# Kernel tuning notes

Hardware: AMD Instinct MI355X
Metric: run time of the kernel (lower is better)

## Reference

```python
import jax, jax.numpy as jnp
import numpy as np

B, IN, FS, S, H = 4096, 4096, 4096, 64, 512  # batch, input_size, first_size, shape_lstm, n_hidden
D = FS // S  # per-step feature for left/right (=64); up/down per-step feature = S (=64)


def _lstm_cell(x, h, c, Wih, Whh, bih, bhh):
    # standard torch LSTMCell gate order: i, f, g, o
    g = x @ Wih.T + bih + h @ Whh.T + bhh  # (B, 4H)
    i, f, gg, o = jnp.split(g, 4, axis=-1)
    c = jax.nn.sigmoid(f) * c + jax.nn.sigmoid(i) * jnp.tanh(gg)
    h = jax.nn.sigmoid(o) * jnp.tanh(c)
    return h, c


def setup_inputs() -> dict:
    key = jax.random.key(0)
    ks = jax.random.split(key, 20)
    def cell(k, d_in):
        k1, k2, k3, k4 = jax.random.split(k, 4)
        s = 1.0 / np.sqrt(H)
        return (jax.random.uniform(k1, (4 * H, d_in), jnp.float32, -s, s),
                jax.random.uniform(k2, (4 * H, H), jnp.float32, -s, s),
                jax.random.uniform(k3, (4 * H,), jnp.float32, -s, s),
                jax.random.uniform(k4, (4 * H,), jnp.float32, -s, s))
    Wih_l, Whh_l, bih_l, bhh_l = cell(ks[0], D)
    Wih_r, Whh_r, bih_r, bhh_r = cell(ks[1], D)
    Wih_d, Whh_d, bih_d, bhh_d = cell(ks[2], S)
    return {
        "x": jax.random.normal(ks[3], (B, IN), jnp.float32),
        "h0": jax.random.normal(ks[4], (4, B, H), jnp.float32),
        "c0": jax.random.normal(ks[5], (4, B, H), jnp.float32),
        "W1": jax.random.normal(ks[6], (FS, IN), jnp.float32) * (1.0 / np.sqrt(IN)),
        "b1": jnp.zeros((FS,), jnp.float32),
        "Wih_l": Wih_l, "Whh_l": Whh_l, "bih_l": bih_l, "bhh_l": bhh_l,
        "Wih_r": Wih_r, "Whh_r": Whh_r, "bih_r": bih_r, "bhh_r": bhh_r,
        "Wih_d": Wih_d, "Whh_d": Whh_d, "bih_d": bih_d, "bhh_d": bhh_d,
        "W3": jax.random.normal(ks[7], (10, 4 * H), jnp.float32) * (1.0 / np.sqrt(4 * H)),
        "b3": jnp.zeros((10,), jnp.float32),
    }


def reference(x, h0, c0, W1, b1, Wih_l, Whh_l, bih_l, bhh_l,
              Wih_r, Whh_r, bih_r, bhh_r, Wih_d, Whh_d, bih_d, bhh_d, W3, b3):
    feat = jax.nn.relu(x @ W1.T + b1)            # (B, FS); dropout=identity (eval)
    il = feat.reshape(B, S, D)
    x_left = jnp.transpose(il, (1, 0, 2))         # (S, B, D)
    x_right = x_left[::-1]
    x_up = jnp.transpose(il, (2, 0, 1))           # (D, B, S); loop uses first S steps
    x_down = x_up[::-1]

    def step(carry, xs):
        (hl, cl, hr, cr, hu, cu, hd, cd) = carry
        xl, xr, xu, xd = xs
        hl, cl = _lstm_cell(xl, hl, cl, Wih_l, Whh_l, bih_l, bhh_l)
        hr, cr = _lstm_cell(xr, hr, cr, Wih_r, Whh_r, bih_r, bhh_r)
        # original code uses the DOWN cell for both up and down directions
        hu, cu = _lstm_cell(xu, hu, cu, Wih_d, Whh_d, bih_d, bhh_d)
        hd, cd = _lstm_cell(xd, hd, cd, Wih_d, Whh_d, bih_d, bhh_d)
        return (hl, cl, hr, cr, hu, cu, hd, cd), None

    carry0 = (h0[0], c0[0], h0[1], c0[1], h0[2], c0[2], h0[3], c0[3])
    (hl, _, hr, _, hu, _, hd, _), _ = jax.lax.scan(
        step, carry0, (x_left[:S], x_right[:S], x_up[:S], x_down[:S]))
    out = jnp.concatenate([hl, hr, hu, hd], axis=1)  # (B, 4H)
    logits = out @ W3.T + b3
    return jax.nn.log_softmax(logits, axis=1)
```

## Files before the change

### kernel.cpp

```cpp
#include <hip/hip_runtime.h>
#include <cstddef>
#include <cstdint>

namespace {

constexpr int kB  = 4096;
constexpr int kIN = 4096;
constexpr int kFS = 4096;
constexpr int kS  = 64;
constexpr int kH  = 512;
constexpr int kNG = 2048;
constexpr int kKC = 576;
constexpr int kKTiles = kKC / 32;

typedef __bf16 bf16_t;
typedef __bf16 bfrag  __attribute__((ext_vector_type(8)));
typedef __bf16 bf16v4 __attribute__((ext_vector_type(4)));
typedef float  f32x4  __attribute__((ext_vector_type(4)));

__device__ __forceinline__ void gload16(const void* g, void* l) {
  __builtin_amdgcn_global_load_lds(
      (const __attribute__((address_space(1))) void*)g,
      (__attribute__((address_space(3))) void*)l, 16, 0, 0);
}

__device__ __forceinline__ float sigf(float x) { return 1.0f / (1.0f + __expf(-x)); }
__device__ __forceinline__ float tanh_fast(float x) {
  float e = __expf(2.0f * x);
  return 1.0f - 2.0f / (e + 1.0f);
}


__global__ __launch_bounds__(256) void f2b4_kernel(const float* __restrict__ in,
                                                   bf16_t* __restrict__ out, int n4) {
  int i = blockIdx.x * 256 + threadIdx.x;
  if (i >= n4) return;
  float4 v = reinterpret_cast<const float4*>(in)[i];
  bf16v4 o = {(bf16_t)v.x, (bf16_t)v.y, (bf16_t)v.z, (bf16_t)v.w};
  *reinterpret_cast<bf16v4*>(out + (size_t)i * 4) = o;
}

__global__ __launch_bounds__(256) void pack_wcat_kernel(
    const float* __restrict__ Wih_l, const float* __restrict__ Whh_l,
    const float* __restrict__ Wih_r, const float* __restrict__ Whh_r,
    const float* __restrict__ Wih_d, const float* __restrict__ Whh_d,
    bf16_t* __restrict__ wcat) {
  int idx = blockIdx.x * 256 + threadIdx.x;
  if (idx >= 3 * kNG * kKC) return;
  int m = idx / (kNG * kKC);
  int rem = idx - m * (kNG * kKC);
  int rr = rem / kKC;
  int k  = rem - rr * kKC;
  int u = rr >> 2, g = rr & 3;
  int orow = g * kH + u;
  const float* Wih = (m == 0) ? Wih_l : (m == 1) ? Wih_r : Wih_d;
  const float* Whh = (m == 0) ? Whh_l : (m == 1) ? Whh_r : Whh_d;
  float v = (k < 64) ? Wih[(size_t)orow * 64 + k] : Whh[(size_t)orow * 512 + (k - 64)];
  wcat[idx] = (bf16_t)v;
}

__global__ __launch_bounds__(256) void pack_bias_kernel(
    const float* __restrict__ bih_l, const float* __restrict__ bhh_l,
    const float* __restrict__ bih_r, const float* __restrict__ bhh_r,
    const float* __restrict__ bih_d, const float* __restrict__ bhh_d,
    float* __restrict__ biasc) {
  int idx = blockIdx.x * 256 + threadIdx.x;
  if (idx >= 3 * kNG) return;
  int m = idx / kNG;
  int rr = idx - m * kNG;
  int u = rr >> 2, g = rr & 3;
  int orow = g * kH + u;
  const float* bi = (m == 0) ? bih_l : (m == 1) ? bih_r : bih_d;
  const float* bh = (m == 0) ? bhh_l : (m == 1) ? bhh_r : bhh_d;
  biasc[idx] = bi[orow] + bh[orow];
}

__global__ __launch_bounds__(256) void pack_hc_kernel(const float* __restrict__ h0,
                                                      const float* __restrict__ c0,
                                                      bf16_t* __restrict__ hbuf0,
                                                      float* __restrict__ cbuf, int n) {
  int i = blockIdx.x * 256 + threadIdx.x;
  if (i >= n) return;
  hbuf0[i] = (bf16_t)h0[i];
  cbuf[i]  = c0[i];
}

__global__ __launch_bounds__(256) void transpose64_kernel(const bf16_t* __restrict__ feat,
                                                          bf16_t* __restrict__ featT) {
  __shared__ bf16_t tile[64][65];
  const int b = blockIdx.x;
  const bf16_t* src = feat + (size_t)b * kFS;
  bf16_t* dst = featT + (size_t)b * kFS;
  for (int i = threadIdx.x; i < 4096; i += 256) tile[i >> 6][i & 63] = src[i];
  __syncthreads();
  for (int i = threadIdx.x; i < 4096; i += 256) dst[i] = tile[i & 63][i >> 6];
}


__global__ __launch_bounds__(256, 4) void gemm_feat_kernel(
    const bf16_t* __restrict__ X, const bf16_t* __restrict__ W,
    const float* __restrict__ b1, bf16_t* __restrict__ feat) {
  __shared__ bf16_t As[128 * 32];
  __shared__ bf16_t Bs[128 * 32];
  const int t = threadIdx.x;
  const int bid = blockIdx.x;
  const int widx = (bid & 7) * 128 + (bid >> 3);
  const int bm = widx & 31, bn = widx >> 5;
  const int w = t >> 6, l = t & 63;
  const int wm = (w >> 1) * 64, wn = (w & 1) * 64;
  const int sr = t >> 2;
  const int skS = ((t & 3) ^ ((t >> 3) & 3)) * 8;
  const int lr = l & 15;
  const int lkS = ((l >> 4) ^ ((l >> 1) & 3)) * 8;
  const int lrow4 = (l >> 4) * 4;

  f32x4 acc[4][4];
#pragma unroll
  for (int i = 0; i < 4; ++i)
#pragma unroll
    for (int j = 0; j < 4; ++j) acc[i][j] = (f32x4){0.f, 0.f, 0.f, 0.f};

  const bf16_t* ga = X + (size_t)(bm * 128 + sr) * kIN + skS;
  const bf16_t* gb = W + (size_t)(bn * 128 + sr) * kIN + skS;
  bf16_t* lA = As + w * 512;
  bf16_t* lB = Bs + w * 512;

  for (int kt = 0; kt < kIN / 32; ++kt) {
    gload16(ga, lA);
    gload16(ga + (size_t)64 * kIN, lA + 2048);
    gload16(gb, lB);
    gload16(gb + (size_t)64 * kIN, lB + 2048);
    ga += 32; gb += 32;
    __syncthreads();
    bfrag a[4], b[4];
#pragma unroll
    for (int mi = 0; mi < 4; ++mi)
      a[mi] = *reinterpret_cast<const bfrag*>(&As[(wm + mi * 16 + lr) * 32 + lkS]);
#pragma unroll
    for (int ni = 0; ni < 4; ++ni)
      b[ni] = *reinterpret_cast<const bfrag*>(&Bs[(wn + ni * 16 + lr) * 32 + lkS]);
#pragma unroll
    for (int mi = 0; mi < 4; ++mi)
#pragma unroll
      for (int ni = 0; ni < 4; ++ni)
        acc[mi][ni] = __builtin_amdgcn_mfma_f32_16x16x32_bf16(a[mi], b[ni], acc[mi][ni], 0, 0, 0);
    __syncthreads();
  }

#pragma unroll
  for (int ni = 0; ni < 4; ++ni) {
    const int col = bn * 128 + wn + ni * 16 + lr;
    const float bb = b1[col];
#pragma unroll
    for (int mi = 0; mi < 4; ++mi) {
#pragma unroll
      for (int r = 0; r < 4; ++r) {
        const int row = bm * 128 + wm + mi * 16 + lrow4 + r;
        float v = acc[mi][ni][r] + bb;
        feat[(size_t)row * kFS + col] = (bf16_t)fmaxf(v, 0.0f);
      }
    }
  }
}


__global__ __launch_bounds__(256, 4) void lstm_step_kernel(
    const bf16_t* __restrict__ feat, const bf16_t* __restrict__ featT,
    const bf16_t* __restrict__ wcat, const float* __restrict__ biasc,
    const bf16_t* __restrict__ hin, bf16_t* __restrict__ hout,
    float* __restrict__ cbuf, int s) {
  __shared__ __align__(16) unsigned char smem[32 * 132 * 4];
  bf16_t* As = (bf16_t*)smem;
  bf16_t* Bs = (bf16_t*)(smem + 8192);
  float*  Gs = (float*)smem;

  const int t = threadIdx.x;
  const int bid = blockIdx.x;
  const int widx = (bid & 7) * 256 + (bid >> 3);
  const int cell = widx >> 9;
  const int rwk  = widx & 511;
  const int bm = rwk >> 4, bn = rwk & 15;
  const int w = t >> 6, l = t & 63;
  const int wm = (w >> 1) * 64, wn = (w & 1) * 64;
  const int sr = t >> 2;
  const int skS = ((t & 3) ^ ((t >> 3) & 3)) * 8;
  const int lr = l & 15;
  const int lkS = ((l >> 4) ^ ((l >> 1) & 3)) * 8;
  const int lrow4 = (l >> 4) * 4;

  const bf16_t* xsrc = (cell < 2) ? feat : featT;
  const int off = ((cell & 1) ? (63 - s) : s) * 64;
  const int mat = (cell < 2) ? cell : 2;
  const bf16_t* Wm = wcat + (size_t)mat * kNG * kKC;
  const bf16_t* hc = hin + (size_t)cell * kB * kH;

  f32x4 acc[4][4];
#pragma unroll
  for (int i = 0; i < 4; ++i)
#pragma unroll
    for (int j = 0; j < 4; ++j) acc[i][j] = (f32x4){0.f, 0.f, 0.f, 0.f};

  const bf16_t* gax = xsrc + (size_t)(bm * 128 + sr) * kFS + off + skS;
  const bf16_t* gah = hc + (size_t)(bm * 128 + sr) * kH + skS;
  const bf16_t* gb  = Wm + (size_t)(bn * 128 + sr) * kKC + skS;
  bf16_t* lA = As + w * 512;
  bf16_t* lB = Bs + w * 512;

  for (int kt = 0; kt < kKTiles; ++kt) {
    if (kt < 2) {
      const bf16_t* ga = gax + kt * 32;
      gload16(ga, lA);
      gload16(ga + (size_t)64 * kFS, lA + 2048);
    } else {
      const bf16_t* ga = gah + (kt - 2) * 32;
      gload16(ga, lA);
      gload16(ga + (size_t)64 * kH, lA + 2048);
    }
    gload16(gb, lB);
    gload16(gb + (size_t)64 * kKC, lB + 2048);
    gb += 32;
    __syncthreads();
    bfrag a[4], b[4];
#pragma unroll
    for (int mi = 0; mi < 4; ++mi)
      a[mi] = *reinterpret_cast<const bfrag*>(&As[(wm + mi * 16 + lr) * 32 + lkS]);
#pragma unroll
    for (int ni = 0; ni < 4; ++ni)
      b[ni] = *reinterpret_cast<const bfrag*>(&Bs[(wn + ni * 16 + lr) * 32 + lkS]);
#pragma unroll
    for (int mi = 0; mi < 4; ++mi)
#pragma unroll
      for (int ni = 0; ni < 4; ++ni)
        acc[mi][ni] = __builtin_amdgcn_mfma_f32_16x16x32_bf16(a[mi], b[ni], acc[mi][ni], 0, 0, 0);
    __syncthreads();
  }

  const float* biasn = biasc + mat * kNG + bn * 128;
#pragma unroll
  for (int pass = 0; pass < 4; ++pass) {
    const int half = pass >> 1;
    const int mlo  = (pass & 1) * 2;
    if ((w >> 1) == half) {
#pragma unroll
      for (int ni = 0; ni < 4; ++ni) {
        const int colL = wn + ni * 16 + lr;
        const float bb = biasn[colL];
#pragma unroll
        for (int mi = mlo; mi < mlo + 2; ++mi)
#pragma unroll
          for (int r = 0; r < 4; ++r)
            Gs[((mi - mlo) * 16 + lrow4 + r) * 132 + colL] = acc[mi][ni][r] + bb;
      }
    }
    __syncthreads();
#pragma unroll
    for (int it = 0; it < 4; ++it) {
      const int ci = it * 256 + t;
      const int rowL = ci >> 5;
      const int u = ci & 31;
      const float4 g4 = *reinterpret_cast<const float4*>(&Gs[rowL * 132 + u * 4]);
      const float iv = sigf(g4.x);
      const float fv = sigf(g4.y);
      const float gv = tanh_fast(g4.z);
      const float ov = sigf(g4.w);
      const int batch = bm * 128 + half * 64 + mlo * 16 + rowL;
      const int unit = bn * 32 + u;
      const size_t cidx = ((size_t)cell * kB + batch) * kH + unit;
      const float cn = fv * cbuf[cidx] + iv * gv;
      cbuf[cidx] = cn;
      hout[cidx] = (bf16_t)(ov * tanh_fast(cn));
    }
    __syncthreads();
  }
}


__global__ __launch_bounds__(256) void head_kernel(const bf16_t* __restrict__ hfin,
                                                   const float* __restrict__ W3,
                                                   const float* __restrict__ b3,
                                                   float* __restrict__ out) {
  const int b = blockIdx.x, t = threadIdx.x;
  float acc[10];
#pragma unroll
  for (int j = 0; j < 10; ++j) acc[j] = 0.f;
  for (int k = t; k < 2048; k += 256) {
    const int cell = k >> 9, u = k & 511;
    const float hv = (float)hfin[((size_t)cell * kB + b) * kH + u];
#pragma unroll
    for (int j = 0; j < 10; ++j) acc[j] += hv * W3[j * 2048 + k];
  }
  __shared__ float red[256];
  __shared__ float logits[10];
  for (int j = 0; j < 10; ++j) {
    red[t] = acc[j];
    __syncthreads();
    for (int o2 = 128; o2 > 0; o2 >>= 1) {
      if (t < o2) red[t] += red[t + o2];
      __syncthreads();
    }
    if (t == 0) logits[j] = red[0] + b3[j];
    __syncthreads();
  }
  if (t == 0) {
    float mx = logits[0];
    for (int j = 1; j < 10; ++j) mx = fmaxf(mx, logits[j]);
    float se = 0.f;
    for (int j = 0; j < 10; ++j) se += expf(logits[j] - mx);
    const float lse = mx + logf(se);
    for (int j = 0; j < 10; ++j) out[(size_t)b * 10 + j] = logits[j] - lse;
  }
}

}

extern "C" void kernel_launch(void* const* d_in, const int* in_sizes, int n_in,
                              void* d_out, int out_size, void* d_ws, size_t ws_size,
                              hipStream_t stream) {
  const float* x     = (const float*)d_in[0];
  const float* h0    = (const float*)d_in[1];
  const float* c0    = (const float*)d_in[2];
  const float* W1    = (const float*)d_in[3];
  const float* b1    = (const float*)d_in[4];
  const float* Wih_l = (const float*)d_in[5];
  const float* Whh_l = (const float*)d_in[6];
  const float* bih_l = (const float*)d_in[7];
  const float* bhh_l = (const float*)d_in[8];
  const float* Wih_r = (const float*)d_in[9];
  const float* Whh_r = (const float*)d_in[10];
  const float* bih_r = (const float*)d_in[11];
  const float* bhh_r = (const float*)d_in[12];
  const float* Wih_d = (const float*)d_in[13];
  const float* Whh_d = (const float*)d_in[14];
  const float* bih_d = (const float*)d_in[15];
  const float* bhh_d = (const float*)d_in[16];
  const float* W3    = (const float*)d_in[17];
  const float* b3    = (const float*)d_in[18];
  float* out = (float*)d_out;

  char* p = (char*)d_ws;
  auto take = [&](size_t bytes) {
    char* r = p;
    p += (bytes + 255) & ~(size_t)255;
    return r;
  };
  bf16_t* xb    = (bf16_t*)take((size_t)kB * kIN * 2);
  bf16_t* w1b   = (bf16_t*)take((size_t)kFS * kIN * 2);
  bf16_t* feat  = (bf16_t*)take((size_t)kB * kFS * 2);
  bf16_t* wcat  = (bf16_t*)take((size_t)3 * kNG * kKC * 2);
  float*  biasc = (float*)take((size_t)3 * kNG * 4);
  float*  cbuf  = (float*)take((size_t)4 * kB * kH * 4);
  bf16_t* featT = xb;
  bf16_t* hbuf  = w1b;
  const size_t HSZ = (size_t)4 * kB * kH;

  f2b4_kernel<<<(kB * kIN / 4) / 256, 256, 0, stream>>>(x, xb, kB * kIN / 4);
  f2b4_kernel<<<(kFS * kIN / 4) / 256, 256, 0, stream>>>(W1, w1b, kFS * kIN / 4);
  gemm_feat_kernel<<<dim3(1024), 256, 0, stream>>>(xb, w1b, b1, feat);
  transpose64_kernel<<<kB, 256, 0, stream>>>(feat, featT);
  pack_wcat_kernel<<<(3 * kNG * kKC + 255) / 256, 256, 0, stream>>>(
      Wih_l, Whh_l, Wih_r, Whh_r, Wih_d, Whh_d, wcat);
  pack_bias_kernel<<<(3 * kNG + 255) / 256, 256, 0, stream>>>(
      bih_l, bhh_l, bih_r, bhh_r, bih_d, bhh_d, biasc);
  pack_hc_kernel<<<(int)(HSZ / 256), 256, 0, stream>>>(h0, c0, hbuf, cbuf, (int)HSZ);

  for (int s = 0; s < 64; ++s) {
    lstm_step_kernel<<<dim3(2048), 256, 0, stream>>>(
        feat, featT, wcat, biasc,
        hbuf + (size_t)(s & 1) * HSZ, hbuf + (size_t)((s + 1) & 1) * HSZ, cbuf, s);
  }
  head_kernel<<<kB, 256, 0, stream>>>(hbuf, W3, b3, out);
}
```

Measured before the change: 4.383 ms.

## Rewrite LSTM step GEMM as 256x256 tile with double-buffered LDS pipeline

Replaces the 128x128-tile, 256-thread LSTM step kernel with a 512-thread, 256x256-tile kernel. It uses K=64 slices held in double-buffered dynamic LDS (128 KB) and interleaves async global-to-LDS loads with MFMA phases, controlled by explicit waitcnt, barriers and setprio. The larger tile is meant to cut redundant weight and h traffic and hide load latency behind compute. The gate epilogue now runs per wave without block syncs. In exchange, the grid drops to 512 blocks with at most 2 per CU, and the hand-tuned vmcnt counts are fragile.

Result: faster. 4.151 ms (-5.3%).

```diff
diff --git a/kernel.cpp b/kernel.cpp
--- a/kernel.cpp
+++ b/kernel.cpp
@@ -11,7 +11,6 @@
 constexpr int kH  = 512;
 constexpr int kNG = 2048;
 constexpr int kKC = 576;
-constexpr int kKTiles = kKC / 32;
 
 typedef __bf16 bf16_t;
 typedef __bf16 bfrag  __attribute__((ext_vector_type(8)));
@@ -28,6 +27,17 @@
 __device__ __forceinline__ float tanh_fast(float x) {
   float e = __expf(2.0f * x);
   return 1.0f - 2.0f / (e + 1.0f);
+}
+
+__device__ __forceinline__ f32x4 mfma16(bfrag a, bfrag b, f32x4 c) {
+  return __builtin_amdgcn_mfma_f32_16x16x32_bf16(a, b, c, 0, 0, 0);
+}
+
+__device__ __forceinline__ void vwait(const int n) {
+  if (n == 6)      asm volatile("s_waitcnt vmcnt(6)" ::: "memory");
+  else if (n == 4) asm volatile("s_waitcnt vmcnt(4)" ::: "memory");
+  else             asm volatile("s_waitcnt vmcnt(0)" ::: "memory");
+  __builtin_amdgcn_sched_barrier(0);
 }
 
 
@@ -164,29 +174,129 @@
 }
 
 
-__global__ __launch_bounds__(256, 4) void lstm_step_kernel(
+template <class F1, class F2, class F3, class F4>
+__device__ __forceinline__ void run_tile(
+    const bf16_t* __restrict__ As_, const bf16_t* __restrict__ Bs_,
+    f32x4 (&acc)[8][4], const int wr, const int wc, const int lr, const int lq,
+    F1&& st1, F2&& st2, F3&& st3, F4&& st4,
+    const int v1, const int v2, const int v3, const int v4) {
+  bfrag a[8], b[8];
+  const int sx = lr & 7;
+
+#pragma unroll
+  for (int mm = 0; mm < 4; ++mm)
+#pragma unroll
+    for (int kk = 0; kk < 2; ++kk)
+      a[mm * 2 + kk] = *reinterpret_cast<const bfrag*>(
+          As_ + (wr * 128 + mm * 16 + lr) * 64 + (((kk * 4 + lq) ^ sx) * 8));
+#pragma unroll
+  for (int nn = 0; nn < 2; ++nn)
+#pragma unroll
+    for (int kk = 0; kk < 2; ++kk)
+      b[nn * 2 + kk] = *reinterpret_cast<const bfrag*>(
+          Bs_ + (wc * 64 + nn * 16 + lr) * 64 + (((kk * 4 + lq) ^ sx) * 8));
+  st1();
+  __builtin_amdgcn_s_barrier();
+  asm volatile("s_waitcnt lgkmcnt(0)" ::: "memory");
+  __builtin_amdgcn_sched_barrier(0);
+  __builtin_amdgcn_s_setprio(1);
+#pragma unroll
+  for (int kk = 0; kk < 2; ++kk)
+#pragma unroll
+    for (int mm = 0; mm < 4; ++mm)
+#pragma unroll
+      for (int nn = 0; nn < 2; ++nn)
+        acc[mm][nn] = mfma16(a[mm * 2 + kk], b[nn * 2 + kk], acc[mm][nn]);
+  __builtin_amdgcn_s_setprio(0);
+  __builtin_amdgcn_sched_barrier(0);
+  vwait(v1);
+  __builtin_amdgcn_s_barrier();
+
+#pragma unroll
+  for (int nn = 0; nn < 2; ++nn)
+#pragma unroll
+    for (int kk = 0; kk < 2; ++kk)
+      b[4 + nn * 2 + kk] = *reinterpret_cast<const bfrag*>(
+          Bs_ + (wc * 64 + 32 + nn * 16 + lr) * 64 + (((kk * 4 + lq) ^ sx) * 8));
+  st2();
+  __builtin_amdgcn_s_barrier();
+  asm volatile("s_waitcnt lgkmcnt(0)" ::: "memory");
+  __builtin_amdgcn_sched_barrier(0);
+  __builtin_amdgcn_s_setprio(1);
+#pragma unroll
+  for (int kk = 0; kk < 2; ++kk)
+#pragma unroll
+    for (int mm = 0; mm < 4; ++mm)
+#pragma unroll
+      for (int nn = 0; nn < 2; ++nn)
+        acc[mm][2 + nn] = mfma16(a[mm * 2 + kk], b[4 + nn * 2 + kk], acc[mm][2 + nn]);
+  __builtin_amdgcn_s_setprio(0);
+  __builtin_amdgcn_sched_barrier(0);
+  vwait(v2);
+  __builtin_amdgcn_s_barrier();
+
+#pragma unroll
+  for (int mm = 0; mm < 4; ++mm)
+#pragma unroll
+    for (int kk = 0; kk < 2; ++kk)
+      a[mm * 2 + kk] = *reinterpret_cast<const bfrag*>(
+          As_ + (wr * 128 + 64 + mm * 16 + lr) * 64 + (((kk * 4 + lq) ^ sx) * 8));
+  st3();
+  __builtin_amdgcn_s_barrier();
+  asm volatile("s_waitcnt lgkmcnt(0)" ::: "memory");
+  __builtin_amdgcn_sched_barrier(0);
+  __builtin_amdgcn_s_setprio(1);
+#pragma unroll
+  for (int kk = 0; kk < 2; ++kk)
+#pragma unroll
+    for (int mm = 0; mm < 4; ++mm)
+#pragma unroll
+      for (int nn = 0; nn < 2; ++nn)
+        acc[4 + mm][nn] = mfma16(a[mm * 2 + kk], b[nn * 2 + kk], acc[4 + mm][nn]);
+  __builtin_amdgcn_s_setprio(0);
+  __builtin_amdgcn_sched_barrier(0);
+  vwait(v3);
+  __builtin_amdgcn_s_barrier();
+
+  st4();
+  __builtin_amdgcn_s_barrier();
+  asm volatile("s_waitcnt lgkmcnt(0)" ::: "memory");
+  __builtin_amdgcn_sched_barrier(0);
+  __builtin_amdgcn_s_setprio(1);
+#pragma unroll
+  for (int kk = 0; kk < 2; ++kk)
+#pragma unroll
+    for (int mm = 0; mm < 4; ++mm)
+#pragma unroll
+      for (int nn = 0; nn < 2; ++nn)
+        acc[4 + mm][2 + nn] = mfma16(a[mm * 2 + kk], b[4 + nn * 2 + kk], acc[4 + mm][2 + nn]);
+  __builtin_amdgcn_s_setprio(0);
+  __builtin_amdgcn_sched_barrier(0);
+  vwait(v4);
+  __builtin_amdgcn_s_barrier();
+}
+
+__global__ __launch_bounds__(512, 2) void lstm_step256_kernel(
     const bf16_t* __restrict__ feat, const bf16_t* __restrict__ featT,
     const bf16_t* __restrict__ wcat, const float* __restrict__ biasc,
     const bf16_t* __restrict__ hin, bf16_t* __restrict__ hout,
     float* __restrict__ cbuf, int s) {
-  __shared__ __align__(16) unsigned char smem[32 * 132 * 4];
-  bf16_t* As = (bf16_t*)smem;
-  bf16_t* Bs = (bf16_t*)(smem + 8192);
-  float*  Gs = (float*)smem;
+  extern __shared__ __align__(16) char smem[];
+  bf16_t* Ab[2] = {(bf16_t*)smem, (bf16_t*)(smem + 65536)};
+  bf16_t* Bb[2] = {(bf16_t*)(smem + 32768), (bf16_t*)(smem + 98304)};
 
   const int t = threadIdx.x;
+  const int l = t & 63, w = t >> 6;
+  const int wr = w >> 2, wc = w & 3;
+  const int lr = l & 15, lq = l >> 4;
+  const int srow = l >> 3;
+  const int sslot = (l & 7) ^ srow;
+
   const int bid = blockIdx.x;
-  const int widx = (bid & 7) * 256 + (bid >> 3);
-  const int cell = widx >> 9;
-  const int rwk  = widx & 511;
-  const int bm = rwk >> 4, bn = rwk & 15;
-  const int w = t >> 6, l = t & 63;
-  const int wm = (w >> 1) * 64, wn = (w & 1) * 64;
-  const int sr = t >> 2;
-  const int skS = ((t & 3) ^ ((t >> 3) & 3)) * 8;
-  const int lr = l & 15;
-  const int lkS = ((l >> 4) ^ ((l >> 1) & 3)) * 8;
-  const int lrow4 = (l >> 4) * 4;
+  const int widx = (bid & 7) * 64 + (bid >> 3);
+  const int cell = widx >> 7;
+  const int rwk = widx & 127;
+  const int bm = rwk >> 3, bn = rwk & 7;
 
   const bf16_t* xsrc = (cell < 2) ? feat : featT;
   const int off = ((cell & 1) ? (63 - s) : s) * 64;
@@ -194,83 +304,93 @@
   const bf16_t* Wm = wcat + (size_t)mat * kNG * kKC;
   const bf16_t* hc = hin + (size_t)cell * kB * kH;
 
-  f32x4 acc[4][4];
-#pragma unroll
-  for (int i = 0; i < 4; ++i)
+  auto stage_A = [&](int kt, bf16_t* dstA, int ra) {
+#pragma unroll
+    for (int j = 0; j < 2; ++j) {
+      const int row0 = ra * 64 + w * 8 + j * 128;
+      bf16_t* dst = dstA + row0 * 64;
+      const bf16_t* src = (kt == 0)
+          ? xsrc + (size_t)(bm * 256 + row0 + srow) * kFS + off + sslot * 8
+          : hc + (size_t)(bm * 256 + row0 + srow) * kH + (kt - 1) * 64 + sslot * 8;
+      gload16(src, dst);
+    }
+  };
+  auto stage_B = [&](int kt, bf16_t* dstB, int rb) {
+#pragma unroll
+    for (int j = 0; j < 2; ++j) {
+      const int row0 = (w >> 2) * 64 + (w & 3) * 8 + rb * 32 + j * 128;
+      bf16_t* dst = dstB + row0 * 64;
+      const bf16_t* src =
+          Wm + (size_t)(bn * 256 + row0 + srow) * kKC + kt * 64 + sslot * 8;
+      gload16(src, dst);
+    }
+  };
+
+  f32x4 acc[8][4];
+#pragma unroll
+  for (int i = 0; i < 8; ++i)
 #pragma unroll
     for (int j = 0; j < 4; ++j) acc[i][j] = (f32x4){0.f, 0.f, 0.f, 0.f};
 
-  const bf16_t* gax = xsrc + (size_t)(bm * 128 + sr) * kFS + off + skS;
-  const bf16_t* gah = hc + (size_t)(bm * 128 + sr) * kH + skS;
-  const bf16_t* gb  = Wm + (size_t)(bn * 128 + sr) * kKC + skS;
-  bf16_t* lA = As + w * 512;
-  bf16_t* lB = Bs + w * 512;
-
-  for (int kt = 0; kt < kKTiles; ++kt) {
-    if (kt < 2) {
-      const bf16_t* ga = gax + kt * 32;
-      gload16(ga, lA);
-      gload16(ga + (size_t)64 * kFS, lA + 2048);
-    } else {
-      const bf16_t* ga = gah + (kt - 2) * 32;
-      gload16(ga, lA);
-      gload16(ga + (size_t)64 * kH, lA + 2048);
-    }
-    gload16(gb, lB);
-    gload16(gb + (size_t)64 * kKC, lB + 2048);
-    gb += 32;
-    __syncthreads();
-    bfrag a[4], b[4];
-#pragma unroll
-    for (int mi = 0; mi < 4; ++mi)
-      a[mi] = *reinterpret_cast<const bfrag*>(&As[(wm + mi * 16 + lr) * 32 + lkS]);
-#pragma unroll
-    for (int ni = 0; ni < 4; ++ni)
-      b[ni] = *reinterpret_cast<const bfrag*>(&Bs[(wn + ni * 16 + lr) * 32 + lkS]);
-#pragma unroll
-    for (int mi = 0; mi < 4; ++mi)
-#pragma unroll
-      for (int ni = 0; ni < 4; ++ni)
-        acc[mi][ni] = __builtin_amdgcn_mfma_f32_16x16x32_bf16(a[mi], b[ni], acc[mi][ni], 0, 0, 0);
-    __syncthreads();
-  }
-
-  const float* biasn = biasc + mat * kNG + bn * 128;
-#pragma unroll
-  for (int pass = 0; pass < 4; ++pass) {
-    const int half = pass >> 1;
-    const int mlo  = (pass & 1) * 2;
-    if ((w >> 1) == half) {
-#pragma unroll
-      for (int ni = 0; ni < 4; ++ni) {
-        const int colL = wn + ni * 16 + lr;
-        const float bb = biasn[colL];
-#pragma unroll
-        for (int mi = mlo; mi < mlo + 2; ++mi)
-#pragma unroll
-          for (int r = 0; r < 4; ++r)
-            Gs[((mi - mlo) * 16 + lrow4 + r) * 132 + colL] = acc[mi][ni][r] + bb;
-      }
-    }
-    __syncthreads();
-#pragma unroll
-    for (int it = 0; it < 4; ++it) {
-      const int ci = it * 256 + t;
-      const int rowL = ci >> 5;
-      const int u = ci & 31;
-      const float4 g4 = *reinterpret_cast<const float4*>(&Gs[rowL * 132 + u * 4]);
+  stage_A(0, Ab[0], 0); stage_B(0, Bb[0], 0);
+  stage_A(0, Ab[0], 1); stage_B(0, Bb[0], 1);
+  stage_A(1, Ab[1], 0); stage_B(1, Bb[1], 0);
+  vwait(4);
+  __builtin_amdgcn_s_barrier();
+
+  run_tile(Ab[0], Bb[0], acc, wr, wc, lr, lq,
+           [&] { stage_A(1, Ab[1], 1); }, [&] { stage_B(1, Bb[1], 1); },
+           [&] { stage_A(2, Ab[0], 0); }, [&] { stage_B(2, Bb[0], 0); },
+           6, 6, 6, 6);
+
+  for (int S = 1; S <= 5; S += 2) {
+    run_tile(Ab[1], Bb[1], acc, wr, wc, lr, lq,
+             [&] { stage_A(S + 1, Ab[0], 1); }, [&] { stage_B(S + 1, Bb[0], 1); },
+             [&] { stage_A(S + 2, Ab[1], 0); }, [&] { stage_B(S + 2, Bb[1], 0); },
+             6, 6, 6, 6);
+    run_tile(Ab[0], Bb[0], acc, wr, wc, lr, lq,
+             [&] { stage_A(S + 2, Ab[1], 1); }, [&] { stage_B(S + 2, Bb[1], 1); },
+             [&] { stage_A(S + 3, Ab[0], 0); }, [&] { stage_B(S + 3, Bb[0], 0); },
+             6, 6, 6, 6);
+  }
+  run_tile(Ab[1], Bb[1], acc, wr, wc, lr, lq,
+           [&] { stage_A(8, Ab[0], 1); }, [&] { stage_B(8, Bb[0], 1); },
+           [&] {}, [&] {}, 6, 6, 6, 4);
+  run_tile(Ab[0], Bb[0], acc, wr, wc, lr, lq,
+           [&] {}, [&] {}, [&] {}, [&] {}, 0, 0, 0, 0);
+
+  float* Gw = (float*)smem + w * 2176;
+  const float* biasn = biasc + mat * kNG + bn * 256 + wc * 64;
+  float bb[4];
+#pragma unroll
+  for (int n = 0; n < 4; ++n) bb[n] = biasn[n * 16 + lr];
+  const int rowg0 = bm * 256 + wr * 128;
+  const int unit = bn * 64 + wc * 16 + lr;
+#pragma unroll
+  for (int ch = 0; ch < 4; ++ch) {
+#pragma unroll
+    for (int mm = 0; mm < 2; ++mm) {
+      const int m = ch * 2 + mm;
+#pragma unroll
+      for (int n = 0; n < 4; ++n)
+#pragma unroll
+        for (int j = 0; j < 4; ++j)
+          Gw[(mm * 16 + lq * 4 + j) * 68 + n * 16 + lr] = acc[m][n][j] + bb[n];
+    }
+#pragma unroll
+    for (int rr = 0; rr < 8; ++rr) {
+      const int row = rr * 4 + lq;
+      const float4 g4 = *reinterpret_cast<const float4*>(&Gw[row * 68 + lr * 4]);
       const float iv = sigf(g4.x);
       const float fv = sigf(g4.y);
       const float gv = tanh_fast(g4.z);
       const float ov = sigf(g4.w);
-      const int batch = bm * 128 + half * 64 + mlo * 16 + rowL;
-      const int unit = bn * 32 + u;
-      const size_t cidx = ((size_t)cell * kB + batch) * kH + unit;
+      const int grow = rowg0 + ch * 32 + row;
+      const size_t cidx = ((size_t)cell * kB + grow) * kH + unit;
       const float cn = fv * cbuf[cidx] + iv * gv;
       cbuf[cidx] = cn;
       hout[cidx] = (bf16_t)(ov * tanh_fast(cn));
     }
-    __syncthreads();
   }
 }
 
@@ -353,6 +473,9 @@
   bf16_t* hbuf  = w1b;
   const size_t HSZ = (size_t)4 * kB * kH;
 
+  (void)hipFuncSetAttribute(reinterpret_cast<const void*>(&lstm_step256_kernel),
+                            hipFuncAttributeMaxDynamicSharedMemorySize, 131072);
+
   f2b4_kernel<<<(kB * kIN / 4) / 256, 256, 0, stream>>>(x, xb, kB * kIN / 4);
   f2b4_kernel<<<(kFS * kIN / 4) / 256, 256, 0, stream>>>(W1, w1b, kFS * kIN / 4);
   gemm_feat_kernel<<<dim3(1024), 256, 0, stream>>>(xb, w1b, b1, feat);
@@ -364,7 +487,7 @@
   pack_hc_kernel<<<(int)(HSZ / 256), 256, 0, stream>>>(h0, c0, hbuf, cbuf, (int)HSZ);
 
   for (int s = 0; s < 64; ++s) {
-    lstm_step_kernel<<<dim3(2048), 256, 0, stream>>>(
+    lstm_step256_kernel<<<dim3(512), 512, 131072, stream>>>(
         feat, featT, wcat, biasc,
         hbuf + (size_t)(s & 1) * HSZ, hbuf + (size_t)((s + 1) & 1) * HSZ, cbuf, s);
   }
```

## Double-buffer LSTM step GEMM with 64-wide K tiles and per-wave epilogue

Applied to the files above, without the earlier changes.

The LSTM step kernel now stages 64-wide K tiles into two 32KB LDS buffers, so the next tile's global-to-LDS loads run during the current tile's MFMAs. This halves the number of K iterations and barriers, and raises MFMA priority with setprio. The gate epilogue now goes through a per-wave LDS region instead of four block-wide passes with syncs. The head kernel's reduction is replaced with wave shuffles. The cost is 64KB of dynamic LDS per block, which lowers occupancy to about 2 blocks per CU.

Result: faster. 4.118 ms (-6.1%).

```diff
diff --git a/kernel.cpp b/kernel.cpp
--- a/kernel.cpp
+++ b/kernel.cpp
@@ -11,7 +11,6 @@
 constexpr int kH  = 512;
 constexpr int kNG = 2048;
 constexpr int kKC = 576;
-constexpr int kKTiles = kKC / 32;
 
 typedef __bf16 bf16_t;
 typedef __bf16 bfrag  __attribute__((ext_vector_type(8)));
@@ -28,6 +27,10 @@
 __device__ __forceinline__ float tanh_fast(float x) {
   float e = __expf(2.0f * x);
   return 1.0f - 2.0f / (e + 1.0f);
+}
+
+__device__ __forceinline__ f32x4 mfma16(bfrag a, bfrag b, f32x4 c) {
+  return __builtin_amdgcn_mfma_f32_16x16x32_bf16(a, b, c, 0, 0, 0);
 }
 
 
@@ -164,29 +167,26 @@
 }
 
 
-__global__ __launch_bounds__(256, 4) void lstm_step_kernel(
+__global__ __launch_bounds__(256, 2) void lstm_step128_kernel(
     const bf16_t* __restrict__ feat, const bf16_t* __restrict__ featT,
     const bf16_t* __restrict__ wcat, const float* __restrict__ biasc,
     const bf16_t* __restrict__ hin, bf16_t* __restrict__ hout,
     float* __restrict__ cbuf, int s) {
-  __shared__ __align__(16) unsigned char smem[32 * 132 * 4];
-  bf16_t* As = (bf16_t*)smem;
-  bf16_t* Bs = (bf16_t*)(smem + 8192);
-  float*  Gs = (float*)smem;
+  extern __shared__ __align__(16) char smem[];
 
   const int t = threadIdx.x;
+  const int l = t & 63, w = t >> 6;
+  const int wm = (w >> 1) * 64, wn = (w & 1) * 64;
+  const int lr = l & 15, lq = l >> 4;
+  const int sx = lr & 7;
+  const int srow = l >> 3;
+  const int sslot = (l & 7) ^ srow;
+
   const int bid = blockIdx.x;
   const int widx = (bid & 7) * 256 + (bid >> 3);
   const int cell = widx >> 9;
-  const int rwk  = widx & 511;
+  const int rwk = widx & 511;
   const int bm = rwk >> 4, bn = rwk & 15;
-  const int w = t >> 6, l = t & 63;
-  const int wm = (w >> 1) * 64, wn = (w & 1) * 64;
-  const int sr = t >> 2;
-  const int skS = ((t & 3) ^ ((t >> 3) & 3)) * 8;
-  const int lr = l & 15;
-  const int lkS = ((l >> 4) ^ ((l >> 1) & 3)) * 8;
-  const int lrow4 = (l >> 4) * 4;
 
   const bf16_t* xsrc = (cell < 2) ? feat : featT;
   const int off = ((cell & 1) ? (63 - s) : s) * 64;
@@ -194,83 +194,101 @@
   const bf16_t* Wm = wcat + (size_t)mat * kNG * kKC;
   const bf16_t* hc = hin + (size_t)cell * kB * kH;
 
+  auto stage = [&](int kt, int buf) {
+    char* base = smem + buf * 32768;
+#pragma unroll
+    for (int j = 0; j < 4; ++j) {
+      const int row0 = j * 32 + w * 8;
+      bf16_t* dst = (bf16_t*)base + row0 * 64;
+      const bf16_t* src = (kt == 0)
+          ? xsrc + (size_t)(bm * 128 + row0 + srow) * kFS + off + sslot * 8
+          : hc + (size_t)(bm * 128 + row0 + srow) * kH + (kt - 1) * 64 + sslot * 8;
+      gload16(src, dst);
+    }
+#pragma unroll
+    for (int j = 0; j < 4; ++j) {
+      const int row0 = j * 32 + w * 8;
+      bf16_t* dst = (bf16_t*)(base + 16384) + row0 * 64;
+      const bf16_t* src =
+          Wm + (size_t)(bn * 128 + row0 + srow) * kKC + kt * 64 + sslot * 8;
+      gload16(src, dst);
+    }
+  };
+
   f32x4 acc[4][4];
 #pragma unroll
   for (int i = 0; i < 4; ++i)
 #pragma unroll
     for (int j = 0; j < 4; ++j) acc[i][j] = (f32x4){0.f, 0.f, 0.f, 0.f};
 
-  const bf16_t* gax = xsrc + (size_t)(bm * 128 + sr) * kFS + off + skS;
-  const bf16_t* gah = hc + (size_t)(bm * 128 + sr) * kH + skS;
-  const bf16_t* gb  = Wm + (size_t)(bn * 128 + sr) * kKC + skS;
-  bf16_t* lA = As + w * 512;
-  bf16_t* lB = Bs + w * 512;
-
-  for (int kt = 0; kt < kKTiles; ++kt) {
-    if (kt < 2) {
-      const bf16_t* ga = gax + kt * 32;
-      gload16(ga, lA);
-      gload16(ga + (size_t)64 * kFS, lA + 2048);
-    } else {
-      const bf16_t* ga = gah + (kt - 2) * 32;
-      gload16(ga, lA);
-      gload16(ga + (size_t)64 * kH, lA + 2048);
-    }
-    gload16(gb, lB);
-    gload16(gb + (size_t)64 * kKC, lB + 2048);
-    gb += 32;
-    __syncthreads();
-    bfrag a[4], b[4];
+  stage(0, 0);
+  asm volatile("s_waitcnt vmcnt(0)" ::: "memory");
+  __builtin_amdgcn_sched_barrier(0);
+  __builtin_amdgcn_s_barrier();
+
+  for (int kt = 0; kt < 9; ++kt) {
+    const int cur = kt & 1;
+    if (kt < 8) stage(kt + 1, cur ^ 1);
+    const bf16_t* As_ = (const bf16_t*)(smem + cur * 32768);
+    const bf16_t* Bs_ = (const bf16_t*)(smem + cur * 32768 + 16384);
+    bfrag a[8], b[8];
 #pragma unroll
     for (int mi = 0; mi < 4; ++mi)
-      a[mi] = *reinterpret_cast<const bfrag*>(&As[(wm + mi * 16 + lr) * 32 + lkS]);
+#pragma unroll
+      for (int kk = 0; kk < 2; ++kk)
+        a[mi * 2 + kk] = *reinterpret_cast<const bfrag*>(
+            As_ + (wm + mi * 16 + lr) * 64 + (((kk * 4 + lq) ^ sx) * 8));
 #pragma unroll
     for (int ni = 0; ni < 4; ++ni)
-      b[ni] = *reinterpret_cast<const bfrag*>(&Bs[(wn + ni * 16 + lr) * 32 + lkS]);
-#pragma unroll
-    for (int mi = 0; mi < 4; ++mi)
-#pragma unroll
-      for (int ni = 0; ni < 4; ++ni)
-        acc[mi][ni] = __builtin_amdgcn_mfma_f32_16x16x32_bf16(a[mi], b[ni], acc[mi][ni], 0, 0, 0);
-    __syncthreads();
-  }
-
-  const float* biasn = biasc + mat * kNG + bn * 128;
-#pragma unroll
-  for (int pass = 0; pass < 4; ++pass) {
-    const int half = pass >> 1;
-    const int mlo  = (pass & 1) * 2;
-    if ((w >> 1) == half) {
-#pragma unroll
-      for (int ni = 0; ni < 4; ++ni) {
-        const int colL = wn + ni * 16 + lr;
-        const float bb = biasn[colL];
-#pragma unroll
-        for (int mi = mlo; mi < mlo + 2; ++mi)
-#pragma unroll
-          for (int r = 0; r < 4; ++r)
-            Gs[((mi - mlo) * 16 + lrow4 + r) * 132 + colL] = acc[mi][ni][r] + bb;
-      }
-    }
-    __syncthreads();
+#pragma unroll
+      for (int kk = 0; kk < 2; ++kk)
+        b[ni * 2 + kk] = *reinterpret_cast<const bfrag*>(
+            Bs_ + (wn + ni * 16 + lr) * 64 + (((kk * 4 + lq) ^ sx) * 8));
+    __builtin_amdgcn_s_setprio(1);
+#pragma unroll
+    for (int kk = 0; kk < 2; ++kk)
+#pragma unroll
+      for (int mi = 0; mi < 4; ++mi)
+#pragma unroll
+        for (int ni = 0; ni < 4; ++ni)
+          acc[mi][ni] = mfma16(a[mi * 2 + kk], b[ni * 2 + kk], acc[mi][ni]);
+    __builtin_amdgcn_s_setprio(0);
+    __builtin_amdgcn_sched_barrier(0);
+    asm volatile("s_waitcnt vmcnt(0)" ::: "memory");
+    __builtin_amdgcn_sched_barrier(0);
+    __builtin_amdgcn_s_barrier();
+  }
+
+  float* Gw = (float*)(smem + 32768 + w * 4352);
+  const float* biasn = biasc + mat * kNG + bn * 128 + wn;
+  float bb[4];
+#pragma unroll
+  for (int n = 0; n < 4; ++n) bb[n] = biasn[n * 16 + lr];
+  const int rowg0 = bm * 128 + wm;
+  const int unit0 = bn * 32 + (w & 1) * 16;
+#pragma unroll
+  for (int mi = 0; mi < 4; ++mi) {
+#pragma unroll
+    for (int n = 0; n < 4; ++n)
+#pragma unroll
+      for (int j = 0; j < 4; ++j)
+        Gw[(lq * 4 + j) * 68 + n * 16 + lr] = acc[mi][n][j] + bb[n];
 #pragma unroll
     for (int it = 0; it < 4; ++it) {
-      const int ci = it * 256 + t;
-      const int rowL = ci >> 5;
-      const int u = ci & 31;
-      const float4 g4 = *reinterpret_cast<const float4*>(&Gs[rowL * 132 + u * 4]);
+      const int item = it * 64 + l;
+      const int row = item >> 4;
+      const int u = item & 15;
+      const float4 g4 = *reinterpret_cast<const float4*>(&Gw[row * 68 + u * 4]);
       const float iv = sigf(g4.x);
       const float fv = sigf(g4.y);
       const float gv = tanh_fast(g4.z);
       const float ov = sigf(g4.w);
-      const int batch = bm * 128 + half * 64 + mlo * 16 + rowL;
-      const int unit = bn * 32 + u;
-      const size_t cidx = ((size_t)cell * kB + batch) * kH + unit;
+      const int grow = rowg0 + mi * 16 + row;
+      const size_t cidx = ((size_t)cell * kB + grow) * kH + unit0 + u;
       const float cn = fv * cbuf[cidx] + iv * gv;
       cbuf[cidx] = cn;
       hout[cidx] = (bf16_t)(ov * tanh_fast(cn));
     }
-    __syncthreads();
   }
 }
 
@@ -280,6 +298,7 @@
                                                    const float* __restrict__ b3,
                                                    float* __restrict__ out) {
   const int b = blockIdx.x, t = threadIdx.x;
+  const int l = t & 63, w = t >> 6;
   float acc[10];
 #pragma unroll
   for (int j = 0; j < 10; ++j) acc[j] = 0.f;
@@ -289,24 +308,28 @@
 #pragma unroll
     for (int j = 0; j < 10; ++j) acc[j] += hv * W3[j * 2048 + k];
   }
-  __shared__ float red[256];
-  __shared__ float logits[10];
-  for (int j = 0; j < 10; ++j) {
-    red[t] = acc[j];
-    __syncthreads();
-    for (int o2 = 128; o2 > 0; o2 >>= 1) {
-      if (t < o2) red[t] += red[t + o2];
-      __syncthreads();
-    }
-    if (t == 0) logits[j] = red[0] + b3[j];
-    __syncthreads();
-  }
+#pragma unroll
+  for (int j = 0; j < 10; ++j)
+#pragma unroll
+    for (int o = 32; o > 0; o >>= 1) acc[j] += __shfl_down(acc[j], o, 64);
+  __shared__ float wred[4][10];
+  if (l == 0)
+#pragma unroll
+    for (int j = 0; j < 10; ++j) wred[w][j] = acc[j];
+  __syncthreads();
   if (t == 0) {
+    float logits[10];
+#pragma unroll
+    for (int j = 0; j < 10; ++j)
+      logits[j] = wred[0][j] + wred[1][j] + wred[2][j] + wred[3][j] + b3[j];
     float mx = logits[0];
+#pragma unroll
     for (int j = 1; j < 10; ++j) mx = fmaxf(mx, logits[j]);
     float se = 0.f;
+#pragma unroll
     for (int j = 0; j < 10; ++j) se += expf(logits[j] - mx);
     const float lse = mx + logf(se);
+#pragma unroll
     for (int j = 0; j < 10; ++j) out[(size_t)b * 10 + j] = logits[j] - lse;
   }
 }
@@ -353,6 +376,9 @@
   bf16_t* hbuf  = w1b;
   const size_t HSZ = (size_t)4 * kB * kH;
 
+  (void)hipFuncSetAttribute(reinterpret_cast<const void*>(&lstm_step128_kernel),
+                            hipFuncAttributeMaxDynamicSharedMemorySize, 65536);
+
   f2b4_kernel<<<(kB * kIN / 4) / 256, 256, 0, stream>>>(x, xb, kB * kIN / 4);
   f2b4_kernel<<<(kFS * kIN / 4) / 256, 256, 0, stream>>>(W1, w1b, kFS * kIN / 4);
   gemm_feat_kernel<<<dim3(1024), 256, 0, stream>>>(xb, w1b, b1, feat);
@@ -364,7 +390,7 @@
   pack_hc_kernel<<<(int)(HSZ / 256), 256, 0, stream>>>(h0, c0, hbuf, cbuf, (int)HSZ);
 
   for (int s = 0; s < 64; ++s) {
-    lstm_step_kernel<<<dim3(2048), 256, 0, stream>>>(
+    lstm_step128_kernel<<<dim3(2048), 256, 65536, stream>>>(
         feat, featT, wcat, biasc,
         hbuf + (size_t)(s & 1) * HSZ, hbuf + (size_t)((s + 1) & 1) * HSZ, cbuf, s);
   }
```
